# Kernel optimization log

Measured on AMD Instinct MI355X. Metric: run time of the kernel, lower is better.

## Reference

```python
import jax, jax.numpy as jnp
import numpy as np

B, NC, PY, PX = 1, 2, 32, 32
DIM, HEADS = 1024, 16
IMAGE_H = IMAGE_W = 448
FREQ_BASE = 100.0


def _so3_exp(w):
    # w: (..., 3) axis-angle -> (..., 3, 3) rotation (Rodrigues)
    theta = jnp.maximum(jnp.linalg.norm(w, axis=-1, keepdims=True)[..., None], 1e-8)
    wx, wy, wz = w[..., 0], w[..., 1], w[..., 2]
    z = jnp.zeros_like(wx)
    K = jnp.stack([jnp.stack([z, -wz, wy], -1),
                   jnp.stack([wz, z, -wx], -1),
                   jnp.stack([-wy, wx, z], -1)], -2)
    A = jnp.sin(theta) / theta
    Bc = (1.0 - jnp.cos(theta)) / (theta * theta)
    return jnp.eye(3) + A * K + Bc * (K @ K)


def setup_inputs() -> dict:
    key = jax.random.key(0)
    ks = jax.random.split(key, 6)
    N = NC * PY * PX
    x = jax.random.normal(ks[0], (B, N, DIM), jnp.float32)
    # SE(3) camera extrinsics (world-to-camera)
    R = _so3_exp(0.2 * jax.random.normal(ks[1], (B, NC, 3), jnp.float32))
    t = 0.5 * jax.random.normal(ks[2], (B, NC, 3), jnp.float32)
    ext = jnp.zeros((B, NC, 4, 4), jnp.float32)
    ext = ext.at[..., :3, :3].set(R).at[..., :3, 3].set(t).at[..., 3, 3].set(1.0)
    f = 500.0
    Ks = jnp.zeros((B, NC, 3, 3), jnp.float32)
    Ks = (Ks.at[..., 0, 0].set(f).at[..., 1, 1].set(f)
            .at[..., 0, 2].set(IMAGE_W / 2.0).at[..., 1, 2].set(IMAGE_H / 2.0)
            .at[..., 2, 2].set(1.0))
    s = 1.0 / np.sqrt(DIM)
    qkv_w = s * jax.random.normal(ks[3], (3 * DIM, DIM), jnp.float32)
    proj_w = s * jax.random.normal(ks[4], (DIM, DIM), jnp.float32)
    proj_b = jnp.zeros((DIM,), jnp.float32)
    return dict(x=x, extrinsics=ext, Ks=Ks, qkv_w=qkv_w, proj_w=proj_w, proj_b=proj_b,
                image_h=IMAGE_H, image_w=IMAGE_W, patch_h=PY, patch_w=PX)


def _prope_attention(x, extrinsics, Ks, qkv_w, proj_w, proj_b,
                     image_h, image_w, patch_h, patch_w):
    Bb, N, C = x.shape
    H = HEADS
    D = C // H
    nc = extrinsics.shape[1]
    n_per = patch_h * patch_w  # tokens per camera

    # ---- QKV projection ----
    qkv = (x @ qkv_w.T).reshape(Bb, N, 3, H, D).transpose(0, 3, 2, 1, 4)  # B,H,3,N,D
    q, k, v = qkv[:, :, 0], qkv[:, :, 1], qkv[:, :, 2]

    # ---- per-camera normalized projection matrices P = K_norm(4x4) @ viewmat ----
    sx, sy = 2.0 / image_w, 2.0 / image_h  # pixel -> NDC-ish normalization
    Kn = jnp.zeros(Ks.shape[:-2] + (4, 4), x.dtype)
    Kn = (Kn.at[..., 0, 0].set(Ks[..., 0, 0] * sx)
            .at[..., 1, 1].set(Ks[..., 1, 1] * sy)
            .at[..., 0, 2].set(Ks[..., 0, 2] * sx - 1.0)
            .at[..., 1, 2].set(Ks[..., 1, 2] * sy - 1.0)
            .at[..., 2, 2].set(1.0).at[..., 3, 3].set(1.0))
    P = Kn @ extrinsics                      # (B, nc, 4, 4)
    P_inv = jnp.linalg.inv(P)

    def per_token(M):  # (B,nc,4,4) -> (B,N,4,4), broadcast camera over its tokens
        return jnp.repeat(M, n_per, axis=1)

    Mq = per_token(jnp.swapaxes(P_inv, -1, -2))  # P_i^{-T}
    Mk = per_token(P)                            # P_j
    Mo = per_token(P_inv)                        # P_i^{-1}

    # ---- channel split: half projective (blocks of 4), half 2D RoPE ----
    d_proj = D // 2
    d_rope = D - d_proj
    nf = d_rope // 4  # frequencies per axis (pairs of channels)
    freqs = FREQ_BASE ** (-jnp.arange(nf, dtype=x.dtype) / nf)
    ysg, xsg = jnp.meshgrid(jnp.arange(patch_h), jnp.arange(patch_w), indexing='ij')
    pos_x = jnp.tile(xsg.reshape(-1), nc).astype(x.dtype)  # (N,)
    pos_y = jnp.tile(ysg.reshape(-1), nc).astype(x.dtype)
    ang = jnp.concatenate([pos_x[:, None] * freqs, pos_y[:, None] * freqs], -1)  # (N, 2nf)
    cos, sin = jnp.cos(ang), jnp.sin(ang)

    def apply(t, M, sign):
        lead = t.shape[:-1]  # (B,H,N)
        tp = t[..., :d_proj].reshape(lead + (d_proj // 4, 4))
        tp = jnp.einsum('bnij,bhnkj->bhnki', M, tp).reshape(lead + (d_proj,))
        tr = t[..., d_proj:].reshape(lead + (2 * nf, 2))
        a, b = tr[..., 0], tr[..., 1]
        s = sign * sin
        tr = jnp.stack([a * cos - b * s, a * s + b * cos], -1).reshape(lead + (d_rope,))
        return jnp.concatenate([tp, tr], -1)

    q = apply(q, Mq, 1.0)
    k = apply(k, Mk, 1.0)
    v = apply(v, Mk, 1.0)

    # ---- SDPA ----
    scale = 1.0 / np.sqrt(D)
    attn = jax.nn.softmax(jnp.einsum('bhqd,bhkd->bhqk', q, k) * scale, axis=-1)
    out = jnp.einsum('bhqk,bhkd->bhqd', attn, v)

    # ---- inverse output transform ----
    out = apply(out, Mo, -1.0)
    out = out.transpose(0, 2, 1, 3).reshape(Bb, N, C)
    return out @ proj_w.T + proj_b


def reference(x, extrinsics, Ks, qkv_w, proj_w, proj_b, image_h, image_w, patch_h, patch_w):
    return _prope_attention(x, extrinsics, Ks, qkv_w, proj_w, proj_b,
                            image_h, image_w, patch_h, patch_w)
```

## Files before the change

kernel.cpp:

```cpp
#include <hip/hip_runtime.h>
#include <math.h>

#define N_TOK   2048
#define DIM     1024
#define HEADS   16
#define HD      64
#define NCAMS   2
#define NPER    1024
#define DPROJ   32
#define NF      8
#define KSPLIT  2

#define LOG2E   1.44269504088896340736f

typedef _Float16 half8  __attribute__((ext_vector_type(8)));
typedef _Float16 half4h __attribute__((ext_vector_type(4)));
typedef _Float16 half2h __attribute__((ext_vector_type(2)));
typedef __fp16   fp16x2 __attribute__((ext_vector_type(2)));
typedef float    floatx4 __attribute__((ext_vector_type(4)));

#define MATS_OFF  0
#define WPROJ_OFF 256
#define SCR_OFF   (WPROJ_OFF + 524288)
#define XF_OFF    (SCR_OFF)
#define WQKV_OFF  (SCR_OFF + 1048576)
#define OP_OFF    (SCR_OFF + 2621440)
#define ML_OFF    (SCR_OFF + 4718592)
#define Q_OFF     (SCR_OFF + 5767168)
#define K_OFF     (Q_OFF + 1048576)
#define V_OFF     (K_OFF + 1048576)
#define OT_OFF    (V_OFF + 1048576)

__device__ __forceinline__ void gl_lds16(const void* g, void* s) {
    __builtin_amdgcn_global_load_lds((const __attribute__((address_space(1))) void*)g,
                                     (__attribute__((address_space(3))) void*)s, 16, 0, 0);
}

__global__ __launch_bounds__(256) void cast_and_mats(const float* __restrict__ x,
                                                     const float* __restrict__ wqkv,
                                                     const float* __restrict__ wproj,
                                                     const float* __restrict__ ext,
                                                     const float* __restrict__ Ksm,
                                                     _Float16* __restrict__ xf,
                                                     _Float16* __restrict__ wqkvf,
                                                     _Float16* __restrict__ wprojf,
                                                     float* __restrict__ mats) {
    size_t i = ((size_t)blockIdx.x * 256 + threadIdx.x) * 8;
    const float* src; _Float16* dst; size_t off;
    if (i < (size_t)2*1024*1024)       { src = x;     dst = xf;     off = i; }
    else if (i < (size_t)5*1024*1024)  { src = wqkv;  dst = wqkvf;  off = i - (size_t)2*1024*1024; }
    else                               { src = wproj; dst = wprojf; off = i - (size_t)5*1024*1024; }
    float4 a = *(const float4*)(src + off);
    float4 b = *(const float4*)(src + off + 4);
    half8 h;
    h[0] = (_Float16)a.x; h[1] = (_Float16)a.y; h[2] = (_Float16)a.z; h[3] = (_Float16)a.w;
    h[4] = (_Float16)b.x; h[5] = (_Float16)b.y; h[6] = (_Float16)b.z; h[7] = (_Float16)b.w;
    *(half8*)(dst + off) = h;

    if (blockIdx.x == 0 && threadIdx.x < NCAMS) {
        const int c = threadIdx.x;
        const float sx = 2.0f / 448.0f, sy = 2.0f / 448.0f;
        const float* Kc = Ksm + c * 9;
        const float* E  = ext + c * 16;
        float Kn[16];
#pragma unroll
        for (int t = 0; t < 16; t++) Kn[t] = 0.0f;
        Kn[0]  = Kc[0] * sx;
        Kn[2]  = Kc[2] * sx - 1.0f;
        Kn[5]  = Kc[4] * sy;
        Kn[6]  = Kc[5] * sy - 1.0f;
        Kn[10] = 1.0f; Kn[15] = 1.0f;
        float P[16];
#pragma unroll
        for (int r = 0; r < 4; r++)
#pragma unroll
            for (int cc = 0; cc < 4; cc++) {
                float s = 0.0f;
#pragma unroll
                for (int k = 0; k < 4; k++) s += Kn[r*4+k] * E[k*4+cc];
                P[r*4+cc] = s;
            }
        float M[4][8];
        for (int r = 0; r < 4; r++)
            for (int cc = 0; cc < 4; cc++) { M[r][cc] = P[r*4+cc]; M[r][4+cc] = (r==cc) ? 1.0f : 0.0f; }
        for (int col = 0; col < 4; col++) {
            int piv = col;
            for (int r = col+1; r < 4; r++)
                if (fabsf(M[r][col]) > fabsf(M[piv][col])) piv = r;
            if (piv != col)
                for (int j = 0; j < 8; j++) { float tmp = M[col][j]; M[col][j] = M[piv][j]; M[piv][j] = tmp; }
            float d = 1.0f / M[col][col];
            for (int j = 0; j < 8; j++) M[col][j] *= d;
            for (int r = 0; r < 4; r++) {
                if (r == col) continue;
                float f = M[r][col];
                for (int j = 0; j < 8; j++) M[r][j] -= f * M[col][j];
            }
        }
        float Pi[16];
        for (int r = 0; r < 4; r++)
            for (int cc = 0; cc < 4; cc++) Pi[r*4+cc] = M[r][4+cc];
        float* o = mats + c * 48;
        for (int r = 0; r < 4; r++)
            for (int cc = 0; cc < 4; cc++) o[r*4+cc] = Pi[cc*4+r];
        for (int t = 0; t < 16; t++) o[16+t] = P[t];
        for (int t = 0; t < 16; t++) o[32+t] = Pi[t];
    }
}

__global__ __launch_bounds__(256) void gemm_qkv_fused(const _Float16* __restrict__ A,
                                                      const _Float16* __restrict__ Bw,
                                                      const float* __restrict__ mats,
                                                      _Float16* __restrict__ Qf,
                                                      _Float16* __restrict__ Kf,
                                                      _Float16* __restrict__ Vtf) {
    const int Kd = DIM, Nn = 3*DIM;
    __shared__ _Float16 As[2][64 * 32];
    __shared__ _Float16 Bs[2][128 * 32];
    const int tid  = threadIdx.x;
    const int w    = tid >> 6, lane = tid & 63;
    const int ql   = lane & 15, quad = lane >> 4;
    const int lr   = lane >> 2, lc = lane & 3;
    const int row0 = blockIdx.y * 64, col0 = blockIdx.x * 128;

    floatx4 acc[4][2];
#pragma unroll
    for (int mt = 0; mt < 4; mt++)
#pragma unroll
        for (int nt = 0; nt < 2; nt++) acc[mt][nt] = (floatx4){0.f, 0.f, 0.f, 0.f};

    const _Float16* Ab  = A  + (size_t)(row0 + w * 16 + lr) * Kd + lc * 8;
    const _Float16* Bb0 = Bw + (size_t)(col0 + w * 32 + lr) * Kd + lc * 8;
    const _Float16* Bb1 = Bw + (size_t)(col0 + w * 32 + 16 + lr) * Kd + lc * 8;

    gl_lds16(Ab,  &As[0][(w * 16) * 32]);
    gl_lds16(Bb0, &Bs[0][(w * 32) * 32]);
    gl_lds16(Bb1, &Bs[0][(w * 32 + 16) * 32]);

    const int nIter = Kd >> 5;
    for (int i = 0; i < nIter; i++) {
        __syncthreads();
        if (i + 1 < nIter) {
            const int k0 = (i + 1) << 5;
            const int nb = (i + 1) & 1;
            gl_lds16(Ab + k0,  &As[nb][(w * 16) * 32]);
            gl_lds16(Bb0 + k0, &Bs[nb][(w * 32) * 32]);
            gl_lds16(Bb1 + k0, &Bs[nb][(w * 32 + 16) * 32]);
        }
        const int cur = i & 1;
        half8 af[4], bf[2];
#pragma unroll
        for (int mt = 0; mt < 4; mt++)
            af[mt] = *(const half8*)&As[cur][(mt * 16 + ql) * 32 + quad * 8];
#pragma unroll
        for (int nt = 0; nt < 2; nt++)
            bf[nt] = *(const half8*)&Bs[cur][(w * 32 + nt * 16 + ql) * 32 + quad * 8];
#pragma unroll
        for (int mt = 0; mt < 4; mt++)
#pragma unroll
            for (int nt = 0; nt < 2; nt++)
                acc[mt][nt] = __builtin_amdgcn_mfma_f32_16x16x32_f16(af[mt], bf[nt], acc[mt][nt], 0, 0, 0);
    }

    const int s   = col0 >> 10;
    const int cam = row0 >> 10;
    const float* Amat = mats + cam * 48 + (s == 0 ? 0 : 16);
    const int i4 = (ql & 3) * 4;
    const float A0 = Amat[i4+0], A1 = Amat[i4+1], A2 = Amat[i4+2], A3 = Amat[i4+3];
    const int g = lane & ~3;
    const float sc = (s == 0) ? 0.125f * LOG2E : 1.0f;

#pragma unroll
    for (int nt = 0; nt < 2; nt++) {
        const int cb = col0 + w * 32 + nt * 16;
        const int dbase = cb & 63;
        const int d = dbase + ql;
        const int h = (cb >> 6) & 15;
        float out[4][4];
        if (dbase < 32) {
#pragma unroll
            for (int mt = 0; mt < 4; mt++)
#pragma unroll
                for (int r = 0; r < 4; r++) {
                    const float v  = acc[mt][nt][r];
                    const float t0 = __shfl(v, g + 0, 64);
                    const float t1 = __shfl(v, g + 1, 64);
                    const float t2 = __shfl(v, g + 2, 64);
                    const float t3 = __shfl(v, g + 3, 64);
                    out[mt][r] = A0*t0 + A1*t1 + A2*t2 + A3*t3;
                }
        } else {
            const int pt = (d - 32) >> 1;
            const float fr = __expf(-0.5756462732485114f * (float)(pt & 7));
            const bool usex = (pt < NF);
#pragma unroll
            for (int mt = 0; mt < 4; mt++)
#pragma unroll
                for (int r = 0; r < 4; r++) {
                    const float v = acc[mt][nt][r];
                    const float other = __shfl_xor(v, 1, 64);
                    const int n = row0 + mt * 16 + quad * 4 + r;
                    const int p = n & (NPER - 1);
                    const float pos = (float)(usex ? (p & 31) : (p >> 5));
                    float sn, cs; __sincosf(pos * fr, &sn, &cs);
                    const float sgn = (d & 1) ? sn : -sn;
                    out[mt][r] = v * cs + other * sgn;
                }
        }
        if (s < 2) {
            _Float16* dst = (s == 0) ? Qf : Kf;
#pragma unroll
            for (int mt = 0; mt < 4; mt++)
#pragma unroll
                for (int r = 0; r < 4; r++) {
                    const int n = row0 + mt * 16 + quad * 4 + r;
                    dst[((size_t)h * N_TOK + n) * HD + d] = (_Float16)(out[mt][r] * sc);
                }
        } else {
#pragma unroll
            for (int mt = 0; mt < 4; mt++) {
                half4h o4;
#pragma unroll
                for (int r = 0; r < 4; r++) o4[r] = (_Float16)out[mt][r];
                const int n0 = row0 + mt * 16 + quad * 4;
                *(half4h*)&Vtf[((size_t)h * HD + d) * N_TOK + n0] = o4;
            }
        }
    }
}

__global__ __launch_bounds__(256) void gemm_proj(const _Float16* __restrict__ A,
                                                 const _Float16* __restrict__ Bw,
                                                 const float* __restrict__ bias,
                                                 float* __restrict__ C,
                                                 int Nn, int Kd) {
    __shared__ _Float16 As[2][64 * 32];
    __shared__ _Float16 Bs[2][128 * 32];
    const int tid  = threadIdx.x;
    const int w    = tid >> 6, lane = tid & 63;
    const int ql   = lane & 15, quad = lane >> 4;
    const int lr   = lane >> 2, lc = lane & 3;
    const int row0 = blockIdx.y * 64, col0 = blockIdx.x * 128;

    floatx4 acc[4][2];
#pragma unroll
    for (int mt = 0; mt < 4; mt++)
#pragma unroll
        for (int nt = 0; nt < 2; nt++) acc[mt][nt] = (floatx4){0.f, 0.f, 0.f, 0.f};

    const _Float16* Ab  = A  + (size_t)(row0 + w * 16 + lr) * Kd + lc * 8;
    const _Float16* Bb0 = Bw + (size_t)(col0 + w * 32 + lr) * Kd + lc * 8;
    const _Float16* Bb1 = Bw + (size_t)(col0 + w * 32 + 16 + lr) * Kd + lc * 8;

    gl_lds16(Ab,  &As[0][(w * 16) * 32]);
    gl_lds16(Bb0, &Bs[0][(w * 32) * 32]);
    gl_lds16(Bb1, &Bs[0][(w * 32 + 16) * 32]);

    const int nIter = Kd >> 5;
    for (int i = 0; i < nIter; i++) {
        __syncthreads();
        if (i + 1 < nIter) {
            const int k0 = (i + 1) << 5;
            const int nb = (i + 1) & 1;
            gl_lds16(Ab + k0,  &As[nb][(w * 16) * 32]);
            gl_lds16(Bb0 + k0, &Bs[nb][(w * 32) * 32]);
            gl_lds16(Bb1 + k0, &Bs[nb][(w * 32 + 16) * 32]);
        }
        const int cur = i & 1;
        half8 af[4], bf[2];
#pragma unroll
        for (int mt = 0; mt < 4; mt++)
            af[mt] = *(const half8*)&As[cur][(mt * 16 + ql) * 32 + quad * 8];
#pragma unroll
        for (int nt = 0; nt < 2; nt++)
            bf[nt] = *(const half8*)&Bs[cur][(w * 32 + nt * 16 + ql) * 32 + quad * 8];
#pragma unroll
        for (int mt = 0; mt < 4; mt++)
#pragma unroll
            for (int nt = 0; nt < 2; nt++)
                acc[mt][nt] = __builtin_amdgcn_mfma_f32_16x16x32_f16(af[mt], bf[nt], acc[mt][nt], 0, 0, 0);
    }

#pragma unroll
    for (int nt = 0; nt < 2; nt++) {
        const int col = col0 + w * 32 + nt * 16 + ql;
        const float bb = bias[col];
#pragma unroll
        for (int mt = 0; mt < 4; mt++) {
            const int row = row0 + mt * 16 + quad * 4;
#pragma unroll
            for (int r = 0; r < 4; r++)
                C[(size_t)(row + r) * Nn + col] = acc[mt][nt][r] + bb;
        }
    }
}

#define PLD 68
__global__ __launch_bounds__(256) void attn_mfma(const _Float16* __restrict__ Qh,
                                                 const _Float16* __restrict__ Kh,
                                                 const _Float16* __restrict__ Vt,
                                                 _Float16* __restrict__ OP,
                                                 float* __restrict__ ML) {
    __shared__ _Float16 sK[64 * 64];
    __shared__ _Float16 sV[64 * 64];
    __shared__ _Float16 P_lds[4][16][PLD];
    const int w    = threadIdx.x >> 6;
    const int lane = threadIdx.x & 63;
    const int b  = blockIdx.x;
    const int ks = b >> 9;
    const int hh = (b >> 5) & 15;
    const int qb = b & 31;
    const int ql = lane & 15, quad = lane >> 4;
    const int q0 = qb * 64 + w * 16;

    const int srow = lane >> 3;
    const int schk = (lane & 7) ^ srow;
    const int c0 = ((quad ^ (ql & 7)) << 3);
    const int c1 = c0 ^ 32;

    const _Float16* Qp = Qh + ((size_t)hh * N_TOK + q0 + ql) * HD;
    const half8 qf0 = *(const half8*)(Qp + quad * 8);
    const half8 qf1 = *(const half8*)(Qp + 32 + quad * 8);

    const _Float16* Kb = Kh + (size_t)hh * N_TOK * HD;
    const _Float16* Vb = Vt + (size_t)hh * HD * N_TOK;

    floatx4 O[4];
#pragma unroll
    for (int mt = 0; mt < 4; mt++) O[mt] = (floatx4){0.f, 0.f, 0.f, 0.f};
    float m = -1e30f, l = 0.0f;

    const int kstart = ks * (N_TOK / KSPLIT);
    const int nIter  = (N_TOK / KSPLIT) / 64;

    for (int i = 0; i < nIter; i++) {
        const int kb = kstart + i * 64;
#pragma unroll
        for (int j = 0; j < 2; j++) {
            const int r0 = w * 16 + j * 8;
            gl_lds16(Kb + (size_t)(kb + r0 + srow) * HD + schk * 8, &sK[r0 * 64]);
            gl_lds16(Vb + (size_t)(r0 + srow) * N_TOK + kb + schk * 8, &sV[r0 * 64]);
        }
        __syncthreads();
        floatx4 s[4];
#pragma unroll
        for (int kt = 0; kt < 4; kt++) {
            const int rb = (kt * 16 + ql) * 64;
            half8 ka0 = *(const half8*)&sK[rb + c0];
            half8 ka1 = *(const half8*)&sK[rb + c1];
            floatx4 acc = (floatx4){0.f, 0.f, 0.f, 0.f};
            acc = __builtin_amdgcn_mfma_f32_16x16x32_f16(ka0, qf0, acc, 0, 0, 0);
            acc = __builtin_amdgcn_mfma_f32_16x16x32_f16(ka1, qf1, acc, 0, 0, 0);
            s[kt] = acc;
        }
        float bm = -1e30f;
#pragma unroll
        for (int kt = 0; kt < 4; kt++)
#pragma unroll
            for (int r = 0; r < 4; r++) bm = fmaxf(bm, s[kt][r]);
        bm = fmaxf(bm, __shfl_xor(bm, 16, 64));
        bm = fmaxf(bm, __shfl_xor(bm, 32, 64));
        const float mnew = fmaxf(m, bm);
        if (__ballot(bm > m)) {
            const float alpha = exp2f(m - mnew);
            l *= alpha;
#pragma unroll
            for (int mt = 0; mt < 4; mt++)
#pragma unroll
                for (int r = 0; r < 4; r++) O[mt][r] *= alpha;
        }
        m = mnew;
        float p[4][4];
        float ps = 0.0f;
#pragma unroll
        for (int kt = 0; kt < 4; kt++)
#pragma unroll
            for (int r = 0; r < 4; r++) { p[kt][r] = exp2f(s[kt][r] - mnew); ps += p[kt][r]; }
        l += ps;
#pragma unroll
        for (int kt = 0; kt < 4; kt++) {
            union { fp16x2 h; half2h v; } u01, u23;
            u01.h = __builtin_amdgcn_cvt_pkrtz(p[kt][0], p[kt][1]);
            u23.h = __builtin_amdgcn_cvt_pkrtz(p[kt][2], p[kt][3]);
            *(half2h*)&P_lds[w][ql][kt * 16 + quad * 4]     = u01.v;
            *(half2h*)&P_lds[w][ql][kt * 16 + quad * 4 + 2] = u23.v;
        }
        union { half8 v8; half4h v4[2]; } pu0, pu1;
        pu0.v4[0] = *(const half4h*)&P_lds[w][ql][quad * 8];
        pu0.v4[1] = *(const half4h*)&P_lds[w][ql][quad * 8 + 4];
        pu1.v4[0] = *(const half4h*)&P_lds[w][ql][32 + quad * 8];
        pu1.v4[1] = *(const half4h*)&P_lds[w][ql][32 + quad * 8 + 4];
#pragma unroll
        for (int mt = 0; mt < 4; mt++) {
            const int rb = (mt * 16 + ql) * 64;
            half8 va0 = *(const half8*)&sV[rb + c0];
            half8 va1 = *(const half8*)&sV[rb + c1];
            O[mt] = __builtin_amdgcn_mfma_f32_16x16x32_f16(va0, pu0.v8, O[mt], 0, 0, 0);
            O[mt] = __builtin_amdgcn_mfma_f32_16x16x32_f16(va1, pu1.v8, O[mt], 0, 0, 0);
        }
        __syncthreads();
    }
    l += __shfl_xor(l, 16, 64);
    l += __shfl_xor(l, 32, 64);
    const float rl = 1.0f / l;
    _Float16* Op = OP + (((size_t)(ks * HEADS + hh)) * N_TOK + q0 + ql) * HD;
#pragma unroll
    for (int mt = 0; mt < 4; mt++) {
        half4h o4;
#pragma unroll
        for (int r = 0; r < 4; r++) o4[r] = (_Float16)(O[mt][r] * rl);
        *(half4h*)&Op[mt * 16 + quad * 4] = o4;
    }
    if (quad == 0) {
        float2 mlv = {m, l};
        *(float2*)&ML[(((size_t)(ks * HEADS + hh)) * N_TOK + q0 + ql) * 2] = mlv;
    }
}

__global__ __launch_bounds__(256) void transform_out(const _Float16* __restrict__ OP,
                                                     const float* __restrict__ ML,
                                                     const float* __restrict__ mats,
                                                     _Float16* __restrict__ Ot) {
    const int T = blockIdx.x * 256 + threadIdx.x;
    const int sub = T & 7;
    const int h   = (T >> 3) & 15;
    const int n   = T >> 7;

    half8 op[KSPLIT];
    float2 ml[KSPLIT];
#pragma unroll
    for (int i = 0; i < KSPLIT; i++) {
        op[i] = *(const half8*)&OP[(((size_t)(i * HEADS + h)) * N_TOK + n) * HD + sub * 8];
        ml[i] = *(const float2*)&ML[(((size_t)(i * HEADS + h)) * N_TOK + n) * 2];
    }
    float mstar = ml[0].x;
#pragma unroll
    for (int i = 1; i < KSPLIT; i++) mstar = fmaxf(mstar, ml[i].x);
    float W = 0.0f;
    float t[8] = {0.f, 0.f, 0.f, 0.f, 0.f, 0.f, 0.f, 0.f};
#pragma unroll
    for (int i = 0; i < KSPLIT; i++) {
        const float wgt = exp2f(ml[i].x - mstar) * ml[i].y;
        W += wgt;
#pragma unroll
        for (int d = 0; d < 8; d++) t[d] += wgt * (float)op[i][d];
    }
    const float rW = 1.0f / W;
#pragma unroll
    for (int d = 0; d < 8; d++) t[d] *= rW;

    const int cam = n >> 10;
    const float* A = mats + cam * 48 + 32;
    float r[8];
    if (sub < 4) {
#pragma unroll
        for (int g = 0; g < 2; g++)
#pragma unroll
            for (int i = 0; i < 4; i++)
                r[g*4+i] = A[i*4+0]*t[g*4+0] + A[i*4+1]*t[g*4+1]
                         + A[i*4+2]*t[g*4+2] + A[i*4+3]*t[g*4+3];
    } else {
        const int p = n & (NPER - 1);
        const float px = (float)(p & 31), py = (float)(p >> 5);
        const int pt0 = (sub - 4) * 4;
#pragma unroll
        for (int pp = 0; pp < 4; pp++) {
            const int pt = pt0 + pp;
            const float fr = __expf(-0.5756462732485114f * (float)(pt & 7));
            const float ang = (pt < NF ? px : py) * fr;
            float sn, cs; __sincosf(ang, &sn, &cs);
            const float a = t[pp*2], b = t[pp*2+1];
            r[pp*2]   = a * cs + b * sn;
            r[pp*2+1] = -a * sn + b * cs;
        }
    }
    half8 o;
#pragma unroll
    for (int i = 0; i < 8; i++) o[i] = (_Float16)r[i];
    *(half8*)&Ot[(size_t)n * DIM + h * HD + sub * 8] = o;
}

extern "C" void kernel_launch(void* const* d_in, const int* in_sizes, int n_in,
                              void* d_out, int out_size, void* d_ws, size_t ws_size,
                              hipStream_t stream) {
    const float* x      = (const float*)d_in[0];
    const float* ext    = (const float*)d_in[1];
    const float* Ks     = (const float*)d_in[2];
    const float* qkv_w  = (const float*)d_in[3];
    const float* proj_w = (const float*)d_in[4];
    const float* proj_b = (const float*)d_in[5];
    float* out = (float*)d_out;

    float* ws   = (float*)d_ws;
    float* mats = ws + MATS_OFF;
    _Float16* Wprojf = (_Float16*)(ws + WPROJ_OFF);
    _Float16* Xf     = (_Float16*)(ws + XF_OFF);
    _Float16* Wqkvf  = (_Float16*)(ws + WQKV_OFF);
    _Float16* OP     = (_Float16*)(ws + OP_OFF);
    float*    ML     = ws + ML_OFF;
    _Float16* Qf  = (_Float16*)(ws + Q_OFF);
    _Float16* Kf  = (_Float16*)(ws + K_OFF);
    _Float16* Vtf = (_Float16*)(ws + V_OFF);
    _Float16* Ot16 = (_Float16*)(ws + OT_OFF);

    cast_and_mats<<<3072, 256, 0, stream>>>(x, qkv_w, proj_w, ext, Ks,
                                            Xf, Wqkvf, Wprojf, mats);

    gemm_qkv_fused<<<dim3(3*DIM/128, N_TOK/64), 256, 0, stream>>>(
        Xf, Wqkvf, mats, Qf, Kf, Vtf);

    attn_mfma<<<KSPLIT * HEADS * (N_TOK / 64), 256, 0, stream>>>(Qf, Kf, Vtf, OP, ML);

    transform_out<<<N_TOK * HEADS * 8 / 256, 256, 0, stream>>>(OP, ML, mats, Ot16);

    gemm_proj<<<dim3(DIM/128, N_TOK/64), 256, 0, stream>>>(
        Ot16, Wprojf, proj_b, out, DIM, DIM);
}
```

Before: 183.5 us.

## Fuse split-K combine and inverse transform into output projection GEMM A-staging

Removes the separate transform_out kernel and its Ot16 intermediate buffer. The output projection GEMM now builds its A tile on the fly: for each K-chunk it loads both split-K partials and their max/sum, merges them, applies the inverse projective/rope transform, and writes fp16 to LDS. This saves one launch and a global write/read of the transformed output. In exchange, each of the 8 column blocks recomputes the combine and transform, and the staging becomes synchronous register loads plus math instead of async global-to-LDS copies, which may stall the GEMM pipeline.

Result: no change. 184.6 us (+0.6%).

```diff
diff --git a/kernel.cpp b/kernel.cpp
--- a/kernel.cpp
+++ b/kernel.cpp
@@ -29,7 +29,6 @@
 #define Q_OFF     (SCR_OFF + 5767168)
 #define K_OFF     (Q_OFF + 1048576)
 #define V_OFF     (K_OFF + 1048576)
-#define OT_OFF    (V_OFF + 1048576)
 
 __device__ __forceinline__ void gl_lds16(const void* g, void* s) {
     __builtin_amdgcn_global_load_lds((const __attribute__((address_space(1))) void*)g,
@@ -114,7 +113,7 @@
                                                       _Float16* __restrict__ Qf,
                                                       _Float16* __restrict__ Kf,
                                                       _Float16* __restrict__ Vtf) {
-    const int Kd = DIM, Nn = 3*DIM;
+    const int Kd = DIM;
     __shared__ _Float16 As[2][64 * 32];
     __shared__ _Float16 Bs[2][128 * 32];
     const int tid  = threadIdx.x;
@@ -225,72 +224,6 @@
                 const int n0 = row0 + mt * 16 + quad * 4;
                 *(half4h*)&Vtf[((size_t)h * HD + d) * N_TOK + n0] = o4;
             }
-        }
-    }
-}
-
-__global__ __launch_bounds__(256) void gemm_proj(const _Float16* __restrict__ A,
-                                                 const _Float16* __restrict__ Bw,
-                                                 const float* __restrict__ bias,
-                                                 float* __restrict__ C,
-                                                 int Nn, int Kd) {
-    __shared__ _Float16 As[2][64 * 32];
-    __shared__ _Float16 Bs[2][128 * 32];
-    const int tid  = threadIdx.x;
-    const int w    = tid >> 6, lane = tid & 63;
-    const int ql   = lane & 15, quad = lane >> 4;
-    const int lr   = lane >> 2, lc = lane & 3;
-    const int row0 = blockIdx.y * 64, col0 = blockIdx.x * 128;
-
-    floatx4 acc[4][2];
-#pragma unroll
-    for (int mt = 0; mt < 4; mt++)
-#pragma unroll
-        for (int nt = 0; nt < 2; nt++) acc[mt][nt] = (floatx4){0.f, 0.f, 0.f, 0.f};
-
-    const _Float16* Ab  = A  + (size_t)(row0 + w * 16 + lr) * Kd + lc * 8;
-    const _Float16* Bb0 = Bw + (size_t)(col0 + w * 32 + lr) * Kd + lc * 8;
-    const _Float16* Bb1 = Bw + (size_t)(col0 + w * 32 + 16 + lr) * Kd + lc * 8;
-
-    gl_lds16(Ab,  &As[0][(w * 16) * 32]);
-    gl_lds16(Bb0, &Bs[0][(w * 32) * 32]);
-    gl_lds16(Bb1, &Bs[0][(w * 32 + 16) * 32]);
-
-    const int nIter = Kd >> 5;
-    for (int i = 0; i < nIter; i++) {
-        __syncthreads();
-        if (i + 1 < nIter) {
-            const int k0 = (i + 1) << 5;
-            const int nb = (i + 1) & 1;
-            gl_lds16(Ab + k0,  &As[nb][(w * 16) * 32]);
-            gl_lds16(Bb0 + k0, &Bs[nb][(w * 32) * 32]);
-            gl_lds16(Bb1 + k0, &Bs[nb][(w * 32 + 16) * 32]);
-        }
-        const int cur = i & 1;
-        half8 af[4], bf[2];
-#pragma unroll
-        for (int mt = 0; mt < 4; mt++)
-            af[mt] = *(const half8*)&As[cur][(mt * 16 + ql) * 32 + quad * 8];
-#pragma unroll
-        for (int nt = 0; nt < 2; nt++)
-            bf[nt] = *(const half8*)&Bs[cur][(w * 32 + nt * 16 + ql) * 32 + quad * 8];
-#pragma unroll
-        for (int mt = 0; mt < 4; mt++)
-#pragma unroll
-            for (int nt = 0; nt < 2; nt++)
-                acc[mt][nt] = __builtin_amdgcn_mfma_f32_16x16x32_f16(af[mt], bf[nt], acc[mt][nt], 0, 0, 0);
-    }
-
-#pragma unroll
-    for (int nt = 0; nt < 2; nt++) {
-        const int col = col0 + w * 32 + nt * 16 + ql;
-        const float bb = bias[col];
-#pragma unroll
-        for (int mt = 0; mt < 4; mt++) {
-            const int row = row0 + mt * 16 + quad * 4;
-#pragma unroll
-            for (int r = 0; r < 4; r++)
-                C[(size_t)(row + r) * Nn + col] = acc[mt][nt][r] + bb;
         }
     }
 }
@@ -417,67 +350,118 @@
     }
 }
 
-__global__ __launch_bounds__(256) void transform_out(const _Float16* __restrict__ OP,
-                                                     const float* __restrict__ ML,
-                                                     const float* __restrict__ mats,
-                                                     _Float16* __restrict__ Ot) {
-    const int T = blockIdx.x * 256 + threadIdx.x;
-    const int sub = T & 7;
-    const int h   = (T >> 3) & 15;
-    const int n   = T >> 7;
-
-    half8 op[KSPLIT];
-    float2 ml[KSPLIT];
-#pragma unroll
-    for (int i = 0; i < KSPLIT; i++) {
-        op[i] = *(const half8*)&OP[(((size_t)(i * HEADS + h)) * N_TOK + n) * HD + sub * 8];
-        ml[i] = *(const float2*)&ML[(((size_t)(i * HEADS + h)) * N_TOK + n) * 2];
-    }
-    float mstar = ml[0].x;
-#pragma unroll
-    for (int i = 1; i < KSPLIT; i++) mstar = fmaxf(mstar, ml[i].x);
-    float W = 0.0f;
-    float t[8] = {0.f, 0.f, 0.f, 0.f, 0.f, 0.f, 0.f, 0.f};
-#pragma unroll
-    for (int i = 0; i < KSPLIT; i++) {
-        const float wgt = exp2f(ml[i].x - mstar) * ml[i].y;
-        W += wgt;
-#pragma unroll
-        for (int d = 0; d < 8; d++) t[d] += wgt * (float)op[i][d];
-    }
-    const float rW = 1.0f / W;
-#pragma unroll
-    for (int d = 0; d < 8; d++) t[d] *= rW;
-
-    const int cam = n >> 10;
-    const float* A = mats + cam * 48 + 32;
-    float r[8];
-    if (sub < 4) {
-#pragma unroll
-        for (int g = 0; g < 2; g++)
-#pragma unroll
-            for (int i = 0; i < 4; i++)
-                r[g*4+i] = A[i*4+0]*t[g*4+0] + A[i*4+1]*t[g*4+1]
-                         + A[i*4+2]*t[g*4+2] + A[i*4+3]*t[g*4+3];
-    } else {
-        const int p = n & (NPER - 1);
-        const float px = (float)(p & 31), py = (float)(p >> 5);
-        const int pt0 = (sub - 4) * 4;
-#pragma unroll
-        for (int pp = 0; pp < 4; pp++) {
-            const int pt = pt0 + pp;
-            const float fr = __expf(-0.5756462732485114f * (float)(pt & 7));
-            const float ang = (pt < NF ? px : py) * fr;
-            float sn, cs; __sincosf(ang, &sn, &cs);
-            const float a = t[pp*2], b = t[pp*2+1];
-            r[pp*2]   = a * cs + b * sn;
-            r[pp*2+1] = -a * sn + b * cs;
-        }
-    }
-    half8 o;
-#pragma unroll
-    for (int i = 0; i < 8; i++) o[i] = (_Float16)r[i];
-    *(half8*)&Ot[(size_t)n * DIM + h * HD + sub * 8] = o;
+__global__ __launch_bounds__(256) void gemm_proj_fused(const _Float16* __restrict__ OP,
+                                                       const float* __restrict__ ML,
+                                                       const float* __restrict__ mats,
+                                                       const _Float16* __restrict__ Bw,
+                                                       const float* __restrict__ bias,
+                                                       float* __restrict__ C) {
+    const int Kd = DIM, Nn = DIM;
+    __shared__ _Float16 As[2][64 * 32];
+    __shared__ _Float16 Bs[2][128 * 32];
+    const int tid  = threadIdx.x;
+    const int w    = tid >> 6, lane = tid & 63;
+    const int ql   = lane & 15, quad = lane >> 4;
+    const int lr   = lane >> 2, lc = lane & 3;
+    const int row0 = blockIdx.y * 64, col0 = blockIdx.x * 128;
+
+    const int n   = row0 + w * 16 + lr;
+    const int cam = row0 >> 10;
+    const float* Ao = mats + cam * 48 + 32;
+    const int p = n & (NPER - 1);
+    const float px = (float)(p & 31), py = (float)(p >> 5);
+
+    floatx4 acc[4][2];
+#pragma unroll
+    for (int mt = 0; mt < 4; mt++)
+#pragma unroll
+        for (int nt = 0; nt < 2; nt++) acc[mt][nt] = (floatx4){0.f, 0.f, 0.f, 0.f};
+
+    const _Float16* Bb0 = Bw + (size_t)(col0 + w * 32 + lr) * Kd + lc * 8;
+    const _Float16* Bb1 = Bw + (size_t)(col0 + w * 32 + 16 + lr) * Kd + lc * 8;
+
+    auto stageA = [&](int k0, _Float16* dstLds) {
+        const int h = k0 >> 6;
+        const int d = (k0 & 32) + lc * 8;
+        float2 ml0 = *(const float2*)&ML[(((size_t)h) * N_TOK + n) * 2];
+        float2 ml1 = *(const float2*)&ML[(((size_t)(HEADS + h)) * N_TOK + n) * 2];
+        half8 op0 = *(const half8*)&OP[(((size_t)h) * N_TOK + n) * HD + d];
+        half8 op1 = *(const half8*)&OP[(((size_t)(HEADS + h)) * N_TOK + n) * HD + d];
+        const float mstar = fmaxf(ml0.x, ml1.x);
+        const float w0 = exp2f(ml0.x - mstar) * ml0.y;
+        const float w1 = exp2f(ml1.x - mstar) * ml1.y;
+        const float rW = 1.0f / (w0 + w1);
+        const float wa = w0 * rW, wb = w1 * rW;
+        float t[8], r[8];
+#pragma unroll
+        for (int j = 0; j < 8; j++) t[j] = wa * (float)op0[j] + wb * (float)op1[j];
+        if (d < 32) {
+#pragma unroll
+            for (int g = 0; g < 2; g++)
+#pragma unroll
+                for (int i = 0; i < 4; i++)
+                    r[g*4+i] = Ao[i*4+0]*t[g*4+0] + Ao[i*4+1]*t[g*4+1]
+                             + Ao[i*4+2]*t[g*4+2] + Ao[i*4+3]*t[g*4+3];
+        } else {
+#pragma unroll
+            for (int pp = 0; pp < 4; pp++) {
+                const int pt = lc * 4 + pp;
+                const float fr = __expf(-0.5756462732485114f * (float)(pt & 7));
+                const float ang = (pt < NF ? px : py) * fr;
+                float sn, cs; __sincosf(ang, &sn, &cs);
+                const float a = t[pp*2], b = t[pp*2+1];
+                r[pp*2]   = a * cs + b * sn;
+                r[pp*2+1] = -a * sn + b * cs;
+            }
+        }
+        union { half8 v8; fp16x2 h2[4]; } o;
+#pragma unroll
+        for (int pp = 0; pp < 4; pp++)
+            o.h2[pp] = __builtin_amdgcn_cvt_pkrtz(r[pp*2], r[pp*2+1]);
+        *(half8*)&dstLds[(w * 16 + lr) * 32 + lc * 8] = o.v8;
+    };
+
+    stageA(0, As[0]);
+    gl_lds16(Bb0, &Bs[0][(w * 32) * 32]);
+    gl_lds16(Bb1, &Bs[0][(w * 32 + 16) * 32]);
+
+    const int nIter = Kd >> 5;
+    for (int i = 0; i < nIter; i++) {
+        __syncthreads();
+        if (i + 1 < nIter) {
+            const int k0 = (i + 1) << 5;
+            const int nb = (i + 1) & 1;
+            stageA(k0, As[nb]);
+            gl_lds16(Bb0 + k0, &Bs[nb][(w * 32) * 32]);
+            gl_lds16(Bb1 + k0, &Bs[nb][(w * 32 + 16) * 32]);
+        }
+        const int cur = i & 1;
+        half8 af[4], bf[2];
+#pragma unroll
+        for (int mt = 0; mt < 4; mt++)
+            af[mt] = *(const half8*)&As[cur][(mt * 16 + ql) * 32 + quad * 8];
+#pragma unroll
+        for (int nt = 0; nt < 2; nt++)
+            bf[nt] = *(const half8*)&Bs[cur][(w * 32 + nt * 16 + ql) * 32 + quad * 8];
+#pragma unroll
+        for (int mt = 0; mt < 4; mt++)
+#pragma unroll
+            for (int nt = 0; nt < 2; nt++)
+                acc[mt][nt] = __builtin_amdgcn_mfma_f32_16x16x32_f16(af[mt], bf[nt], acc[mt][nt], 0, 0, 0);
+    }
+
+#pragma unroll
+    for (int nt = 0; nt < 2; nt++) {
+        const int col = col0 + w * 32 + nt * 16 + ql;
+        const float bb = bias[col];
+#pragma unroll
+        for (int mt = 0; mt < 4; mt++) {
+            const int row = row0 + mt * 16 + quad * 4;
+#pragma unroll
+            for (int r = 0; r < 4; r++)
+                C[(size_t)(row + r) * Nn + col] = acc[mt][nt][r] + bb;
+        }
+    }
 }
 
 extern "C" void kernel_launch(void* const* d_in, const int* in_sizes, int n_in,
@@ -501,7 +485,6 @@
     _Float16* Qf  = (_Float16*)(ws + Q_OFF);
     _Float16* Kf  = (_Float16*)(ws + K_OFF);
     _Float16* Vtf = (_Float16*)(ws + V_OFF);
-    _Float16* Ot16 = (_Float16*)(ws + OT_OFF);
 
     cast_and_mats<<<3072, 256, 0, stream>>>(x, qkv_w, proj_w, ext, Ks,
                                             Xf, Wqkvf, Wprojf, mats);
@@ -511,8 +494,6 @@
 
     attn_mfma<<<KSPLIT * HEADS * (N_TOK / 64), 256, 0, stream>>>(Qf, Kf, Vtf, OP, ML);
 
-    transform_out<<<N_TOK * HEADS * 8 / 256, 256, 0, stream>>>(OP, ML, mats, Ot16);
-
-    gemm_proj<<<dim3(DIM/128, N_TOK/64), 256, 0, stream>>>(
-        Ot16, Wprojf, proj_b, out, DIM, DIM);
-}
+    gemm_proj_fused<<<dim3(DIM/128, N_TOK/64), 256, 0, stream>>>(
+        OP, ML, mats, Wprojf, proj_b, out);
+}
```
